# Kernel optimization log

Measured on AMD Instinct MI355X. Metric: run time of the kernel, lower is better.

Reference implementation:

```python
import jax, jax.numpy as jnp
import numpy as np

NEG_SLOPE = 0.2  # PyG GATConv default


def gat_conv(x, src, dst, W, att_src, att_dst, bias, n_nodes):
    # x: [N, F_in]; W: [F_in, H*C]; att_*: [H, C]; bias: [H*C]
    H, C = att_src.shape
    h = (x @ W).reshape(n_nodes, H, C)                      # [N, H, C]
    a_src = jnp.sum(h * att_src, axis=-1)                   # [N, H]
    a_dst = jnp.sum(h * att_dst, axis=-1)                   # [N, H]
    e = jax.nn.leaky_relu(a_src[src] + a_dst[dst], NEG_SLOPE)  # [E, H]
    # segment softmax over incoming edges of each dst node
    e_max = jax.ops.segment_max(e, dst, num_segments=n_nodes)
    e_max = jnp.where(jnp.isfinite(e_max), e_max, 0.0)
    ex = jnp.exp(e - e_max[dst])                             # [E, H]
    denom = jax.ops.segment_sum(ex, dst, num_segments=n_nodes)
    alpha = ex / (denom[dst] + 1e-16)                        # [E, H]
    msg = h[src] * alpha[:, :, None]                         # [E, H, C]
    out = jax.ops.segment_sum(msg, dst, num_segments=n_nodes)  # [N, H, C]
    return out.reshape(n_nodes, H * C) + bias


def setup_inputs() -> dict:
    key = jax.random.key(0)
    ks = jax.random.split(key, 12)
    N, F_in, Hd, heads, F_out, E = 50000, 128, 32, 8, 16, 800000
    x = jax.random.normal(ks[0], (N, F_in), dtype=jnp.float32)
    edge_index = jax.random.randint(ks[1], (2, E), 0, N, dtype=jnp.int64)
    g = 0.1
    return {
        "x": x,
        "edge_index": edge_index,
        "W1": jax.random.normal(ks[2], (F_in, heads * Hd), dtype=jnp.float32) * g,
        "att_src1": jax.random.normal(ks[3], (heads, Hd), dtype=jnp.float32) * g,
        "att_dst1": jax.random.normal(ks[4], (heads, Hd), dtype=jnp.float32) * g,
        "b1": jnp.zeros((heads * Hd,), dtype=jnp.float32),
        "W2": jax.random.normal(ks[5], (heads * Hd, Hd), dtype=jnp.float32) * g,
        "att_src2": jax.random.normal(ks[6], (1, Hd), dtype=jnp.float32) * g,
        "att_dst2": jax.random.normal(ks[7], (1, Hd), dtype=jnp.float32) * g,
        "b2": jnp.zeros((Hd,), dtype=jnp.float32),
        "Wout": jax.random.normal(ks[8], (Hd, F_out), dtype=jnp.float32) * g,
        "bout": jnp.zeros((F_out,), dtype=jnp.float32),
    }


def reference(x, edge_index, W1, att_src1, att_dst1, b1, W2, att_src2, att_dst2, b2, Wout, bout):
    N = x.shape[0]
    # PyG GATConv adds self loops by default
    loops = jnp.arange(N, dtype=edge_index.dtype)
    src = jnp.concatenate([edge_index[0], loops])
    dst = jnp.concatenate([edge_index[1], loops])
    h = jax.nn.elu(gat_conv(x, src, dst, W1, att_src1, att_dst1, b1, N))
    # dropout is identity in eval mode
    h = jax.nn.elu(gat_conv(h, src, dst, W2, att_src2, att_dst2, b2, N))
    return h @ Wout + bout
```

## Files before the change

kernel.cpp:

```cpp
#include <hip/hip_runtime.h>
#include <math.h>

#define NEG_SLOPE 0.2f

typedef __attribute__((ext_vector_type(8))) short bfrag8;
typedef __attribute__((ext_vector_type(4))) float f4acc;

__device__ __forceinline__ float bflo(unsigned int u) {
  union { unsigned int i; float f; } c;
  c.i = u << 16;
  return c.f;
}
__device__ __forceinline__ float bfhi(unsigned int u) {
  union { unsigned int i; float f; } c;
  c.i = u & 0xFFFF0000u;
  return c.f;
}
__device__ __forceinline__ unsigned short f2bf(float f) {
  union { float f; unsigned int i; } c;
  c.f = f;
  unsigned int i = c.i;
  return (unsigned short)((i + 0x7FFFu + ((i >> 16) & 1u)) >> 16);
}
__device__ __forceinline__ float elu(float x) { return x > 0.f ? x : __expf(x) - 1.f; }


__global__ __launch_bounds__(256) void prep_kernel(const int* __restrict__ ei,
                                                   int* __restrict__ counts,
                                                   const float* __restrict__ x,
                                                   const float* __restrict__ W1,
                                                   const float* __restrict__ W2,
                                                   unsigned short* __restrict__ xb,
                                                   unsigned short* __restrict__ w1t,
                                                   unsigned short* __restrict__ w2t,
                                                   int e, int xThreads, int totalx) {
  int gid = blockIdx.x * 256 + threadIdx.x;
  if (gid < e) {
    atomicAdd(&counts[ei[e + gid]], 1);
    return;
  }
  int g1 = gid - e;
  if (g1 < xThreads) {
    int i = g1 * 8;
    if (i < totalx) {
      float4 v0 = *(const float4*)(x + i);
      float4 v1 = *(const float4*)(x + i + 4);
      uint4 q;
      q.x = (unsigned int)f2bf(v0.x) | ((unsigned int)f2bf(v0.y) << 16);
      q.y = (unsigned int)f2bf(v0.z) | ((unsigned int)f2bf(v0.w) << 16);
      q.z = (unsigned int)f2bf(v1.x) | ((unsigned int)f2bf(v1.y) << 16);
      q.w = (unsigned int)f2bf(v1.z) | ((unsigned int)f2bf(v1.w) << 16);
      *(uint4*)(xb + i) = q;
    }
    return;
  }
  int g2 = g1 - xThreads;
#pragma unroll
  for (int u = 0; u < 4; ++u) {
    int j = g2 * 4 + u;
    if (j < 128 * 256) {
      int k = j >> 8, c = j & 255;
      w1t[c * 128 + k] = f2bf(W1[j]);
    } else if (j < 128 * 256 + 256 * 32) {
      int j2 = j - 128 * 256;
      int k = j2 >> 5, c = j2 & 31;
      w2t[c * 256 + k] = f2bf(W2[j2]);
    }
  }
}


#define SCAN_TILE 2048
__global__ __launch_bounds__(256) void scan_kernel(const int* __restrict__ counts,
                                                   int* __restrict__ offsets,
                                                   int* __restrict__ cursor,
                                                   int* __restrict__ bsum,
                                                   int* __restrict__ done,
                                                   int n, int nb) {
  __shared__ int wtot[4];
  __shared__ int preS, totS;
  int tid = threadIdx.x;
  int b = blockIdx.x;
  int base = b * SCAN_TILE + tid * 8;
  int v[8];
#pragma unroll
  for (int k = 0; k < 8; ++k) v[k] = (base + k < n) ? counts[base + k] + 1 : 0;
#pragma unroll
  for (int k = 1; k < 8; ++k) v[k] += v[k - 1];
  int tsum = v[7];
  int lane = tid & 63, w = tid >> 6;
  int ws = tsum;
#pragma unroll
  for (int off = 1; off < 64; off <<= 1) {
    int t = __shfl_up(ws, off, 64);
    if (lane >= off) ws += t;
  }
  if (lane == 63) wtot[w] = ws;
  __syncthreads();
  int woff = 0;
#pragma unroll
  for (int k = 0; k < 3; ++k)
    if (k < w) woff += wtot[k];
  int thrExcl = woff + ws - tsum;
  int blockTot = wtot[0] + wtot[1] + wtot[2] + wtot[3];

  if (tid == 0) {
    atomicExch(&bsum[b], blockTot);
    atomicAdd(done, 1);
    while (atomicAdd(done, 0) < nb) {
    }
    int pre = 0, tot = 0;
    for (int k = 0; k < nb; ++k) {
      int t = atomicAdd(&bsum[k], 0);
      if (k < b) pre += t;
      tot += t;
    }
    preS = pre;
    totS = tot;
  }
  __syncthreads();
  int pre = preS;
#pragma unroll
  for (int k = 0; k < 8; ++k) {
    int i = base + k;
    if (i < n) {
      int excl = pre + thrExcl + (k ? v[k - 1] : 0);
      offsets[i] = excl;
      cursor[i] = excl;
    }
  }
  if (b == 0 && tid == 0) offsets[n] = totS;
}


__global__ __launch_bounds__(256) void fillgemm1_kernel(
    const int* __restrict__ ei, int* __restrict__ cursor, int* __restrict__ csr,
    const unsigned short* __restrict__ xb, const unsigned short* __restrict__ w1t,
    const float* __restrict__ att_src, const float* __restrict__ att_dst,
    unsigned short* __restrict__ h1b, float* __restrict__ as1, float* __restrict__ ad1,
    int n, int e, int gBlocksX) {
  int bid = blockIdx.x;
  int gBlocks = gBlocksX * 2;
  if (bid >= gBlocks) {
    int i = (bid - gBlocks) * 256 + threadIdx.x;
    if (i < e) {
      int s = ei[i];
      int d = ei[e + i];
      int pos = atomicAdd(&cursor[d], 1);
      csr[pos] = s;
    } else if (i < e + n) {
      int node = i - e;
      int pos = atomicAdd(&cursor[node], 1);
      csr[pos] = node;
    } else if (i < e + n + 64) {
      csr[i] = 0;
    }
    return;
  }
  int bx = bid % gBlocksX, by = bid / gBlocksX;
  int tid = threadIdx.x;
  int wave = tid >> 6, lane = tid & 63;
  int quad = lane >> 4, l16 = lane & 15;
  int row0 = bx * 64 + wave * 16;
  int col0 = by * 128;
  int rowA = min(row0 + l16, n - 1);

  f4acc acc[8];
#pragma unroll
  for (int t = 0; t < 8; ++t) acc[t] = (f4acc)(0.f);

#pragma unroll
  for (int kc = 0; kc < 4; ++kc) {
    bfrag8 a = *(const bfrag8*)(xb + (size_t)rowA * 128 + kc * 32 + quad * 8);
#pragma unroll
    for (int t = 0; t < 8; ++t) {
      bfrag8 b = *(const bfrag8*)(w1t + (size_t)(col0 + t * 16 + l16) * 128 + kc * 32 + quad * 8);
      acc[t] = __builtin_amdgcn_mfma_f32_16x16x32_bf16(a, b, acc[t], 0, 0, 0);
    }
  }

#pragma unroll
  for (int r = 0; r < 4; ++r) {
    int gr = row0 + quad * 4 + r;
    if (gr < n) {
#pragma unroll
      for (int t = 0; t < 8; ++t)
        h1b[(size_t)gr * 256 + col0 + t * 16 + l16] = f2bf(acc[t][r]);
    }
  }

  float s1[4][4], s2[4][4];
#pragma unroll
  for (int r = 0; r < 4; ++r)
#pragma unroll
    for (int hl = 0; hl < 4; ++hl) { s1[r][hl] = 0.f; s2[r][hl] = 0.f; }
#pragma unroll
  for (int t = 0; t < 8; ++t) {
    float av = att_src[col0 + t * 16 + l16];
    float dv = att_dst[col0 + t * 16 + l16];
    int hl = t >> 1;
#pragma unroll
    for (int r = 0; r < 4; ++r) {
      s1[r][hl] += acc[t][r] * av;
      s2[r][hl] += acc[t][r] * dv;
    }
  }
#pragma unroll
  for (int r = 0; r < 4; ++r) {
#pragma unroll
    for (int hl = 0; hl < 4; ++hl) {
      float v1 = s1[r][hl], v2 = s2[r][hl];
      v1 += __shfl_xor(v1, 1); v1 += __shfl_xor(v1, 2);
      v1 += __shfl_xor(v1, 4); v1 += __shfl_xor(v1, 8);
      v2 += __shfl_xor(v2, 1); v2 += __shfl_xor(v2, 2);
      v2 += __shfl_xor(v2, 4); v2 += __shfl_xor(v2, 8);
      if (l16 == 0) {
        int gr = row0 + quad * 4 + r;
        if (gr < n) {
          int hg = (col0 >> 5) + hl;
          as1[(size_t)gr * 8 + hg] = v1;
          ad1[(size_t)gr * 8 + hg] = v2;
        }
      }
    }
  }
}


__global__ __launch_bounds__(256) void agg1_kernel(const unsigned short* __restrict__ h1b,
                                                   const float* __restrict__ as1,
                                                   const float* __restrict__ ad1,
                                                   const int* __restrict__ offsets,
                                                   const int* __restrict__ csr,
                                                   const float* __restrict__ bias,
                                                   unsigned short* __restrict__ h1ob, int n) {
  __shared__ float peLds[4 * 64 * 8];
  int gtid = blockIdx.x * 256 + threadIdx.x;
  int node = gtid >> 6;
  int lane = gtid & 63;
  if (node >= n) return;
  float* myPe = peLds + (threadIdx.x >> 6) * 512;
  int beg = offsets[node], end = offsets[node + 1];
  int deg = end - beg;
  int half = lane >> 5, sub = lane & 31, head = sub >> 2;

  float4 adv0 = ((const float4*)(ad1 + (size_t)node * 8))[0];
  float4 adv1 = ((const float4*)(ad1 + (size_t)node * 8))[1];
  float ad_[8] = {adv0.x, adv0.y, adv0.z, adv0.w, adv1.x, adv1.y, adv1.z, adv1.w};

  float l = 0.f;
  float a[8] = {};

  for (int c0 = 0; c0 < deg; c0 += 64) {
    int cnt = min(64, deg - c0);
    bool valid = (c0 + lane) < deg;
    int sreg = csr[beg + c0 + lane];
    {
      const float4* ap = (const float4*)(as1 + (size_t)sreg * 8);
      float4 r0 = ap[0], r1 = ap[1];
      float asv[8] = {r0.x, r0.y, r0.z, r0.w, r1.x, r1.y, r1.z, r1.w};
      float pv[8];
#pragma unroll
      for (int h = 0; h < 8; ++h) {
        float ev = asv[h] + ad_[h];
        ev = ev > 0.f ? ev : NEG_SLOPE * ev;
        pv[h] = valid ? __expf(ev) : 0.f;
      }
      *(float4*)&myPe[lane * 8 + 0] = make_float4(pv[0], pv[1], pv[2], pv[3]);
      *(float4*)&myPe[lane * 8 + 4] = make_float4(pv[4], pv[5], pv[6], pv[7]);
    }
#pragma unroll 8
    for (int j = 0; j < cnt; j += 2) {
      int e2 = j + half;
      int s2 = __shfl(sreg, e2);
      float pe = myPe[e2 * 8 + head];
      l += pe;
      uint4 hv = *(const uint4*)(h1b + (size_t)s2 * 256 + sub * 8);
      a[0] += pe * bflo(hv.x);
      a[1] += pe * bfhi(hv.x);
      a[2] += pe * bflo(hv.y);
      a[3] += pe * bfhi(hv.y);
      a[4] += pe * bflo(hv.z);
      a[5] += pe * bfhi(hv.z);
      a[6] += pe * bflo(hv.w);
      a[7] += pe * bfhi(hv.w);
    }
  }
  l += __shfl_xor(l, 32);
#pragma unroll
  for (int i = 0; i < 8; ++i) a[i] += __shfl_xor(a[i], 32);

  if (half == 0) {
    float inv = 1.f / (l + 1e-16f);
    const float4* bp = (const float4*)(bias + sub * 8);
    float4 b0 = bp[0], b1 = bp[1];
    float o[8];
    o[0] = elu(a[0] * inv + b0.x);
    o[1] = elu(a[1] * inv + b0.y);
    o[2] = elu(a[2] * inv + b0.z);
    o[3] = elu(a[3] * inv + b0.w);
    o[4] = elu(a[4] * inv + b1.x);
    o[5] = elu(a[5] * inv + b1.y);
    o[6] = elu(a[6] * inv + b1.z);
    o[7] = elu(a[7] * inv + b1.w);
    unsigned int q[4];
#pragma unroll
    for (int j = 0; j < 4; ++j)
      q[j] = (unsigned int)f2bf(o[j * 2]) | ((unsigned int)f2bf(o[j * 2 + 1]) << 16);
    *(uint4*)(h1ob + (size_t)node * 256 + sub * 8) = make_uint4(q[0], q[1], q[2], q[3]);
  }
}


__global__ __launch_bounds__(256) void gemm2_kernel(const unsigned short* __restrict__ h1ob,
                                                    const unsigned short* __restrict__ w2t,
                                                    const float* __restrict__ att_src,
                                                    const float* __restrict__ att_dst,
                                                    unsigned short* __restrict__ h2b,
                                                    float* __restrict__ as2,
                                                    float* __restrict__ ad2, int n) {
  int tid = threadIdx.x;
  int wave = tid >> 6, lane = tid & 63;
  int quad = lane >> 4, l16 = lane & 15;
  int row0 = blockIdx.x * 64 + wave * 16;
  int rowA = min(row0 + l16, n - 1);

  f4acc acc[2];
  acc[0] = (f4acc)(0.f);
  acc[1] = (f4acc)(0.f);

#pragma unroll
  for (int kc = 0; kc < 8; ++kc) {
    bfrag8 a = *(const bfrag8*)(h1ob + (size_t)rowA * 256 + kc * 32 + quad * 8);
#pragma unroll
    for (int t = 0; t < 2; ++t) {
      bfrag8 b = *(const bfrag8*)(w2t + (size_t)(t * 16 + l16) * 256 + kc * 32 + quad * 8);
      acc[t] = __builtin_amdgcn_mfma_f32_16x16x32_bf16(a, b, acc[t], 0, 0, 0);
    }
  }

#pragma unroll
  for (int r = 0; r < 4; ++r) {
    int gr = row0 + quad * 4 + r;
    if (gr < n) {
      h2b[(size_t)gr * 32 + l16] = f2bf(acc[0][r]);
      h2b[(size_t)gr * 32 + 16 + l16] = f2bf(acc[1][r]);
    }
  }

  float s1[4], s2v[4];
#pragma unroll
  for (int r = 0; r < 4; ++r) { s1[r] = 0.f; s2v[r] = 0.f; }
#pragma unroll
  for (int t = 0; t < 2; ++t) {
    float av = att_src[t * 16 + l16];
    float dv = att_dst[t * 16 + l16];
#pragma unroll
    for (int r = 0; r < 4; ++r) {
      s1[r] += acc[t][r] * av;
      s2v[r] += acc[t][r] * dv;
    }
  }
#pragma unroll
  for (int r = 0; r < 4; ++r) {
    float v1 = s1[r], v2 = s2v[r];
    v1 += __shfl_xor(v1, 1); v1 += __shfl_xor(v1, 2);
    v1 += __shfl_xor(v1, 4); v1 += __shfl_xor(v1, 8);
    v2 += __shfl_xor(v2, 1); v2 += __shfl_xor(v2, 2);
    v2 += __shfl_xor(v2, 4); v2 += __shfl_xor(v2, 8);
    if (l16 == 0) {
      int gr = row0 + quad * 4 + r;
      if (gr < n) {
        as2[gr] = v1;
        ad2[gr] = v2;
      }
    }
  }
}


__global__ __launch_bounds__(256) void agg2_kernel(const unsigned short* __restrict__ h2b,
                                                   const float* __restrict__ as2,
                                                   const float* __restrict__ ad2,
                                                   const int* __restrict__ offsets,
                                                   const int* __restrict__ csr,
                                                   const float* __restrict__ bias,
                                                   const float* __restrict__ Wout,
                                                   const float* __restrict__ bout,
                                                   float* __restrict__ out, int n) {
  __shared__ float peLds[4 * 64];
  __shared__ float wLds[512];
  __shared__ float hrow[4][32];
  int tid = threadIdx.x;
  wLds[tid] = Wout[tid];
  wLds[tid + 256] = Wout[tid + 256];
  __syncthreads();

  int gtid = blockIdx.x * 256 + tid;
  int node = gtid >> 6;
  int lane = gtid & 63;
  if (node >= n) return;
  int wv = tid >> 6;
  float* myPe = peLds + wv * 64;
  float ad = ad2[node];
  int beg = offsets[node], end = offsets[node + 1];
  int deg = end - beg;
  int quarter = lane >> 4;
  int dsub = lane & 15;

  float l = 0.f, a0 = 0.f, a1 = 0.f;
  for (int c0 = 0; c0 < deg; c0 += 64) {
    int cnt = min(64, deg - c0);
    bool valid = (c0 + lane) < deg;
    int sreg = csr[beg + c0 + lane];
    float ev = as2[sreg] + ad;
    ev = ev > 0.f ? ev : NEG_SLOPE * ev;
    myPe[lane] = valid ? __expf(ev) : 0.f;
#pragma unroll 8
    for (int j = 0; j < cnt; j += 4) {
      int e2 = j + quarter;
      int s2 = __shfl(sreg, e2);
      float pe = myPe[e2];
      l += pe;
      unsigned int hv = *(const unsigned int*)(h2b + (size_t)s2 * 32 + dsub * 2);
      a0 += pe * bflo(hv);
      a1 += pe * bfhi(hv);
    }
  }
  l += __shfl_xor(l, 16);
  l += __shfl_xor(l, 32);
  a0 += __shfl_xor(a0, 16);
  a1 += __shfl_xor(a1, 16);
  a0 += __shfl_xor(a0, 32);
  a1 += __shfl_xor(a1, 32);
  if (lane < 16) {
    float inv = 1.f / (l + 1e-16f);
    float o0 = elu(a0 * inv + bias[dsub * 2]);
    float o1 = elu(a1 * inv + bias[dsub * 2 + 1]);
    hrow[wv][dsub * 2] = o0;
    hrow[wv][dsub * 2 + 1] = o1;
  }
  if (lane < 16) {
    float s = bout[lane];
#pragma unroll
    for (int c = 0; c < 32; ++c) s += hrow[wv][c] * wLds[c * 16 + lane];
    out[(size_t)node * 16 + lane] = s;
  }
}


extern "C" void kernel_launch(void* const* d_in, const int* in_sizes, int n_in,
                              void* d_out, int out_size, void* d_ws, size_t ws_size,
                              hipStream_t stream) {
  const float* x        = (const float*)d_in[0];
  const int*   ei       = (const int*)d_in[1];
  const float* W1       = (const float*)d_in[2];
  const float* att_src1 = (const float*)d_in[3];
  const float* att_dst1 = (const float*)d_in[4];
  const float* b1       = (const float*)d_in[5];
  const float* W2       = (const float*)d_in[6];
  const float* att_src2 = (const float*)d_in[7];
  const float* att_dst2 = (const float*)d_in[8];
  const float* b2       = (const float*)d_in[9];
  const float* Wout     = (const float*)d_in[10];
  const float* bout     = (const float*)d_in[11];
  float* out = (float*)d_out;

  int n = in_sizes[0] / 128;
  int e = in_sizes[1] / 2;

  char* w = (char*)d_ws;
  unsigned short* h1b  = (unsigned short*)w; w += (size_t)n * 256 * 2;
  unsigned short* h1ob = (unsigned short*)w; w += (size_t)n * 256 * 2;
  unsigned short* xb   = (unsigned short*)w; w += (size_t)n * 128 * 2;
  unsigned short* h2b  = (unsigned short*)w; w += (size_t)n * 32 * 2;
  unsigned short* w1t  = (unsigned short*)w; w += (size_t)256 * 128 * 2;
  unsigned short* w2t  = (unsigned short*)w; w += (size_t)32 * 256 * 2;
  float* as1  = (float*)w; w += (size_t)n * 8 * 4;
  float* ad1  = (float*)w; w += (size_t)n * 8 * 4;
  float* as2  = (float*)w; w += (size_t)n * 4;
  float* ad2  = (float*)w; w += (size_t)n * 4;
  int* counts  = (int*)w; w += (size_t)n * 4;
  int* done    = (int*)w; w += (size_t)16 * 4;
  int* offsets = (int*)w; w += (size_t)(n + 16) * 4;
  int* cursor  = (int*)w; w += (size_t)n * 4;
  int* csr     = (int*)w; w += (size_t)(e + n + 64) * 4;
  int* bsum    = (int*)w; w += (size_t)256 * 4;

  int nb = (n + SCAN_TILE - 1) / SCAN_TILE;

  hipMemsetAsync(counts, 0, (size_t)(n + 16) * 4, stream);

  int xThreads = (n * 128 + 7) / 8;
  int prepThreads = e + xThreads + (128 * 256 + 256 * 32 + 3) / 4;
  prep_kernel<<<(prepThreads + 255) / 256, 256, 0, stream>>>(ei, counts, x, W1, W2,
                                                             xb, w1t, w2t, e, xThreads,
                                                             n * 128);

  scan_kernel<<<nb, 256, 0, stream>>>(counts, offsets, cursor, bsum, done, n, nb);

  int gBlocksX = (n + 63) / 64;
  int gBlocks = gBlocksX * 2;
  int fillBlocks = (e + n + 64 + 255) / 256;
  fillgemm1_kernel<<<gBlocks + fillBlocks, 256, 0, stream>>>(
      ei, cursor, csr, xb, w1t, att_src1, att_dst1, h1b, as1, ad1, n, e, gBlocksX);

  agg1_kernel<<<(n + 3) / 4, 256, 0, stream>>>(h1b, as1, ad1, offsets, csr, b1, h1ob, n);

  gemm2_kernel<<<(n + 63) / 64, 256, 0, stream>>>(h1ob, w2t, att_src2, att_dst2,
                                                  h2b, as2, ad2, n);
  agg2_kernel<<<(n + 3) / 4, 256, 0, stream>>>(h2b, as2, ad2, offsets, csr, b2,
                                               Wout, bout, out, n);
}
```

Before: 336.0 us.

## Fuse layer-2 GEMM into agg1 and convert x to bf16 inside GEMM1

The separate x-to-bf16 pass and the W2 transpose are removed. GEMM1 now reads fp32 x and converts it to bf16 in registers. The layer-2 projection, along with its attention scores, is computed at the end of agg1: each wave stages its ELU output row in LDS and multiplies it by a bf16 copy of W2 held in LDS, so the h1ob intermediate and the gemm2 launch go away. In exchange, every agg1 block reloads and converts all of W2 into LDS, uses more shared memory (which may lower occupancy), and does the 256x32 projection with scalar FMAs instead of MFMA.

```diff
diff --git a/kernel.cpp b/kernel.cpp
--- a/kernel.cpp
+++ b/kernel.cpp
@@ -27,44 +27,21 @@
 
 __global__ __launch_bounds__(256) void prep_kernel(const int* __restrict__ ei,
                                                    int* __restrict__ counts,
-                                                   const float* __restrict__ x,
                                                    const float* __restrict__ W1,
-                                                   const float* __restrict__ W2,
-                                                   unsigned short* __restrict__ xb,
                                                    unsigned short* __restrict__ w1t,
-                                                   unsigned short* __restrict__ w2t,
-                                                   int e, int xThreads, int totalx) {
+                                                   int e) {
   int gid = blockIdx.x * 256 + threadIdx.x;
   if (gid < e) {
     atomicAdd(&counts[ei[e + gid]], 1);
     return;
   }
-  int g1 = gid - e;
-  if (g1 < xThreads) {
-    int i = g1 * 8;
-    if (i < totalx) {
-      float4 v0 = *(const float4*)(x + i);
-      float4 v1 = *(const float4*)(x + i + 4);
-      uint4 q;
-      q.x = (unsigned int)f2bf(v0.x) | ((unsigned int)f2bf(v0.y) << 16);
-      q.y = (unsigned int)f2bf(v0.z) | ((unsigned int)f2bf(v0.w) << 16);
-      q.z = (unsigned int)f2bf(v1.x) | ((unsigned int)f2bf(v1.y) << 16);
-      q.w = (unsigned int)f2bf(v1.z) | ((unsigned int)f2bf(v1.w) << 16);
-      *(uint4*)(xb + i) = q;
-    }
-    return;
-  }
-  int g2 = g1 - xThreads;
+  int g2 = gid - e;
 #pragma unroll
   for (int u = 0; u < 4; ++u) {
     int j = g2 * 4 + u;
     if (j < 128 * 256) {
       int k = j >> 8, c = j & 255;
       w1t[c * 128 + k] = f2bf(W1[j]);
-    } else if (j < 128 * 256 + 256 * 32) {
-      int j2 = j - 128 * 256;
-      int k = j2 >> 5, c = j2 & 31;
-      w2t[c * 256 + k] = f2bf(W2[j2]);
     }
   }
 }
@@ -135,14 +112,13 @@
 
 __global__ __launch_bounds__(256) void fillgemm1_kernel(
     const int* __restrict__ ei, int* __restrict__ cursor, int* __restrict__ csr,
-    const unsigned short* __restrict__ xb, const unsigned short* __restrict__ w1t,
+    const float* __restrict__ x, const unsigned short* __restrict__ w1t,
     const float* __restrict__ att_src, const float* __restrict__ att_dst,
     unsigned short* __restrict__ h1b, float* __restrict__ as1, float* __restrict__ ad1,
-    int n, int e, int gBlocksX) {
+    int n, int e, int fillBlocks, int gBlocksX) {
   int bid = blockIdx.x;
-  int gBlocks = gBlocksX * 2;
-  if (bid >= gBlocks) {
-    int i = (bid - gBlocks) * 256 + threadIdx.x;
+  if (bid < fillBlocks) {
+    int i = bid * 256 + threadIdx.x;
     if (i < e) {
       int s = ei[i];
       int d = ei[e + i];
@@ -157,7 +133,8 @@
     }
     return;
   }
-  int bx = bid % gBlocksX, by = bid / gBlocksX;
+  int gb = bid - fillBlocks;
+  int bx = gb % gBlocksX, by = gb / gBlocksX;
   int tid = threadIdx.x;
   int wave = tid >> 6, lane = tid & 63;
   int quad = lane >> 4, l16 = lane & 15;
@@ -171,7 +148,17 @@
 
 #pragma unroll
   for (int kc = 0; kc < 4; ++kc) {
-    bfrag8 a = *(const bfrag8*)(xb + (size_t)rowA * 128 + kc * 32 + quad * 8);
+    float4 a0 = *(const float4*)(x + (size_t)rowA * 128 + kc * 32 + quad * 8);
+    float4 a1 = *(const float4*)(x + (size_t)rowA * 128 + kc * 32 + quad * 8 + 4);
+    bfrag8 a;
+    a[0] = (short)f2bf(a0.x);
+    a[1] = (short)f2bf(a0.y);
+    a[2] = (short)f2bf(a0.z);
+    a[3] = (short)f2bf(a0.w);
+    a[4] = (short)f2bf(a1.x);
+    a[5] = (short)f2bf(a1.y);
+    a[6] = (short)f2bf(a1.z);
+    a[7] = (short)f2bf(a1.w);
 #pragma unroll
     for (int t = 0; t < 8; ++t) {
       bfrag8 b = *(const bfrag8*)(w1t + (size_t)(col0 + t * 16 + l16) * 128 + kc * 32 + quad * 8);
@@ -233,13 +220,28 @@
                                                    const int* __restrict__ offsets,
                                                    const int* __restrict__ csr,
                                                    const float* __restrict__ bias,
-                                                   unsigned short* __restrict__ h1ob, int n) {
+                                                   const float* __restrict__ W2,
+                                                   const float* __restrict__ att_src2,
+                                                   const float* __restrict__ att_dst2,
+                                                   unsigned short* __restrict__ h2b,
+                                                   float* __restrict__ as2,
+                                                   float* __restrict__ ad2, int n) {
   __shared__ float peLds[4 * 64 * 8];
-  int gtid = blockIdx.x * 256 + threadIdx.x;
+  __shared__ unsigned short w2b[256 * 34];
+  __shared__ float hrow[4][256];
+  int tid = threadIdx.x;
+  for (int t = tid; t < 8192; t += 256) {
+    int c = t >> 5, col = t & 31;
+    w2b[c * 34 + col] = f2bf(W2[t]);
+  }
+  __syncthreads();
+
+  int gtid = blockIdx.x * 256 + tid;
   int node = gtid >> 6;
   int lane = gtid & 63;
   if (node >= n) return;
-  float* myPe = peLds + (threadIdx.x >> 6) * 512;
+  int wv = tid >> 6;
+  float* myPe = peLds + wv * 512;
   int beg = offsets[node], end = offsets[node + 1];
   int deg = end - beg;
   int half = lane >> 5, sub = lane & 31, head = sub >> 2;
@@ -294,86 +296,38 @@
     float inv = 1.f / (l + 1e-16f);
     const float4* bp = (const float4*)(bias + sub * 8);
     float4 b0 = bp[0], b1 = bp[1];
-    float o[8];
-    o[0] = elu(a[0] * inv + b0.x);
-    o[1] = elu(a[1] * inv + b0.y);
-    o[2] = elu(a[2] * inv + b0.z);
-    o[3] = elu(a[3] * inv + b0.w);
-    o[4] = elu(a[4] * inv + b1.x);
-    o[5] = elu(a[5] * inv + b1.y);
-    o[6] = elu(a[6] * inv + b1.z);
-    o[7] = elu(a[7] * inv + b1.w);
-    unsigned int q[4];
-#pragma unroll
-    for (int j = 0; j < 4; ++j)
-      q[j] = (unsigned int)f2bf(o[j * 2]) | ((unsigned int)f2bf(o[j * 2 + 1]) << 16);
-    *(uint4*)(h1ob + (size_t)node * 256 + sub * 8) = make_uint4(q[0], q[1], q[2], q[3]);
-  }
-}
-
-
-__global__ __launch_bounds__(256) void gemm2_kernel(const unsigned short* __restrict__ h1ob,
-                                                    const unsigned short* __restrict__ w2t,
-                                                    const float* __restrict__ att_src,
-                                                    const float* __restrict__ att_dst,
-                                                    unsigned short* __restrict__ h2b,
-                                                    float* __restrict__ as2,
-                                                    float* __restrict__ ad2, int n) {
-  int tid = threadIdx.x;
-  int wave = tid >> 6, lane = tid & 63;
-  int quad = lane >> 4, l16 = lane & 15;
-  int row0 = blockIdx.x * 64 + wave * 16;
-  int rowA = min(row0 + l16, n - 1);
-
-  f4acc acc[2];
-  acc[0] = (f4acc)(0.f);
-  acc[1] = (f4acc)(0.f);
-
-#pragma unroll
-  for (int kc = 0; kc < 8; ++kc) {
-    bfrag8 a = *(const bfrag8*)(h1ob + (size_t)rowA * 256 + kc * 32 + quad * 8);
-#pragma unroll
-    for (int t = 0; t < 2; ++t) {
-      bfrag8 b = *(const bfrag8*)(w2t + (size_t)(t * 16 + l16) * 256 + kc * 32 + quad * 8);
-      acc[t] = __builtin_amdgcn_mfma_f32_16x16x32_bf16(a, b, acc[t], 0, 0, 0);
-    }
-  }
-
-#pragma unroll
-  for (int r = 0; r < 4; ++r) {
-    int gr = row0 + quad * 4 + r;
-    if (gr < n) {
-      h2b[(size_t)gr * 32 + l16] = f2bf(acc[0][r]);
-      h2b[(size_t)gr * 32 + 16 + l16] = f2bf(acc[1][r]);
-    }
-  }
-
-  float s1[4], s2v[4];
-#pragma unroll
-  for (int r = 0; r < 4; ++r) { s1[r] = 0.f; s2v[r] = 0.f; }
-#pragma unroll
-  for (int t = 0; t < 2; ++t) {
-    float av = att_src[t * 16 + l16];
-    float dv = att_dst[t * 16 + l16];
-#pragma unroll
-    for (int r = 0; r < 4; ++r) {
-      s1[r] += acc[t][r] * av;
-      s2v[r] += acc[t][r] * dv;
-    }
-  }
-#pragma unroll
-  for (int r = 0; r < 4; ++r) {
-    float v1 = s1[r], v2 = s2v[r];
-    v1 += __shfl_xor(v1, 1); v1 += __shfl_xor(v1, 2);
-    v1 += __shfl_xor(v1, 4); v1 += __shfl_xor(v1, 8);
-    v2 += __shfl_xor(v2, 1); v2 += __shfl_xor(v2, 2);
-    v2 += __shfl_xor(v2, 4); v2 += __shfl_xor(v2, 8);
-    if (l16 == 0) {
-      int gr = row0 + quad * 4 + r;
-      if (gr < n) {
-        as2[gr] = v1;
-        ad2[gr] = v2;
-      }
+    float* hr = &hrow[wv][sub * 8];
+    hr[0] = elu(a[0] * inv + b0.x);
+    hr[1] = elu(a[1] * inv + b0.y);
+    hr[2] = elu(a[2] * inv + b0.z);
+    hr[3] = elu(a[3] * inv + b0.w);
+    hr[4] = elu(a[4] * inv + b1.x);
+    hr[5] = elu(a[5] * inv + b1.y);
+    hr[6] = elu(a[6] * inv + b1.z);
+    hr[7] = elu(a[7] * inv + b1.w);
+  }
+  int col = lane & 31, ch = lane >> 5;
+  const float* hr = hrow[wv];
+  float v = 0.f;
+  for (int c0 = ch * 128; c0 < ch * 128 + 128; c0 += 8) {
+#pragma unroll
+    for (int k = 0; k < 8; ++k)
+      v += hr[c0 + k] * bflo((unsigned int)w2b[(c0 + k) * 34 + col]);
+  }
+  v += __shfl_xor(v, 32);
+  if (lane < 32) {
+    h2b[(size_t)node * 32 + col] = f2bf(v);
+    float sa = v * att_src2[col];
+    float sd = v * att_dst2[col];
+    sa += __shfl_xor(sa, 1); sa += __shfl_xor(sa, 2);
+    sa += __shfl_xor(sa, 4); sa += __shfl_xor(sa, 8);
+    sa += __shfl_xor(sa, 16);
+    sd += __shfl_xor(sd, 1); sd += __shfl_xor(sd, 2);
+    sd += __shfl_xor(sd, 4); sd += __shfl_xor(sd, 8);
+    sd += __shfl_xor(sd, 16);
+    if (lane == 0) {
+      as2[node] = sa;
+      ad2[node] = sd;
     }
   }
 }
@@ -471,11 +425,8 @@
 
   char* w = (char*)d_ws;
   unsigned short* h1b  = (unsigned short*)w; w += (size_t)n * 256 * 2;
-  unsigned short* h1ob = (unsigned short*)w; w += (size_t)n * 256 * 2;
-  unsigned short* xb   = (unsigned short*)w; w += (size_t)n * 128 * 2;
   unsigned short* h2b  = (unsigned short*)w; w += (size_t)n * 32 * 2;
   unsigned short* w1t  = (unsigned short*)w; w += (size_t)256 * 128 * 2;
-  unsigned short* w2t  = (unsigned short*)w; w += (size_t)32 * 256 * 2;
   float* as1  = (float*)w; w += (size_t)n * 8 * 4;
   float* ad1  = (float*)w; w += (size_t)n * 8 * 4;
   float* as2  = (float*)w; w += (size_t)n * 4;
@@ -491,24 +442,21 @@
 
   hipMemsetAsync(counts, 0, (size_t)(n + 16) * 4, stream);
 
-  int xThreads = (n * 128 + 7) / 8;
-  int prepThreads = e + xThreads + (128 * 256 + 256 * 32 + 3) / 4;
-  prep_kernel<<<(prepThreads + 255) / 256, 256, 0, stream>>>(ei, counts, x, W1, W2,
-                                                             xb, w1t, w2t, e, xThreads,
-                                                             n * 128);
+  int prepThreads = e + (128 * 256 + 3) / 4;
+  prep_kernel<<<(prepThreads + 255) / 256, 256, 0, stream>>>(ei, counts, W1, w1t, e);
 
   scan_kernel<<<nb, 256, 0, stream>>>(counts, offsets, cursor, bsum, done, n, nb);
 
+  int fillBlocks = (e + n + 64 + 255) / 256;
   int gBlocksX = (n + 63) / 64;
-  int gBlocks = gBlocksX * 2;
-  int fillBlocks = (e + n + 64 + 255) / 256;
-  fillgemm1_kernel<<<gBlocks + fillBlocks, 256, 0, stream>>>(
-      ei, cursor, csr, xb, w1t, att_src1, att_dst1, h1b, as1, ad1, n, e, gBlocksX);
-
-  agg1_kernel<<<(n + 3) / 4, 256, 0, stream>>>(h1b, as1, ad1, offsets, csr, b1, h1ob, n);
-
-  gemm2_kernel<<<(n + 63) / 64, 256, 0, stream>>>(h1ob, w2t, att_src2, att_dst2,
-                                                  h2b, as2, ad2, n);
+  int gemmBlocks = gBlocksX * 2;
+  fillgemm1_kernel<<<fillBlocks + gemmBlocks, 256, 0, stream>>>(
+      ei, cursor, csr, x, w1t, att_src1, att_dst1, h1b, as1, ad1, n, e, fillBlocks,
+      gBlocksX);
+
+  agg1_kernel<<<(n + 3) / 4, 256, 0, stream>>>(h1b, as1, ad1, offsets, csr, b1,
+                                               W2, att_src2, att_dst2, h2b, as2, ad2, n);
+
   agg2_kernel<<<(n + 3) / 4, 256, 0, stream>>>(h2b, as2, ad2, offsets, csr, b2,
                                                Wout, bout, out, n);
 }
```

New measurement: 375.5 us. 1.12x slower.

## Convert x to bf16 inside GEMM1, split fill from GEMM, stage h1 stores via LDS

Applied to the files above, without the earlier changes.

Drops the separate x-to-bf16 conversion pass in prep and its workspace buffer, so GEMM1 reads fp32 x directly and converts it in registers. The combined fill+GEMM launch is split into a CSR fill kernel and a standalone 2D-grid GEMM1 kernel. GEMM1 output is staged through shared memory so h1 is written with 16-byte row-contiguous stores instead of scattered 2-byte stores. This trades the extra bf16 copy round trip for double-size x reads in the GEMM, and it gives up the overlap between fill and GEMM in exchange for one more launch.

```diff
diff --git a/kernel.cpp b/kernel.cpp
--- a/kernel.cpp
+++ b/kernel.cpp
@@ -27,34 +27,17 @@
 
 __global__ __launch_bounds__(256) void prep_kernel(const int* __restrict__ ei,
                                                    int* __restrict__ counts,
-                                                   const float* __restrict__ x,
                                                    const float* __restrict__ W1,
                                                    const float* __restrict__ W2,
-                                                   unsigned short* __restrict__ xb,
                                                    unsigned short* __restrict__ w1t,
                                                    unsigned short* __restrict__ w2t,
-                                                   int e, int xThreads, int totalx) {
+                                                   int e) {
   int gid = blockIdx.x * 256 + threadIdx.x;
   if (gid < e) {
     atomicAdd(&counts[ei[e + gid]], 1);
     return;
   }
-  int g1 = gid - e;
-  if (g1 < xThreads) {
-    int i = g1 * 8;
-    if (i < totalx) {
-      float4 v0 = *(const float4*)(x + i);
-      float4 v1 = *(const float4*)(x + i + 4);
-      uint4 q;
-      q.x = (unsigned int)f2bf(v0.x) | ((unsigned int)f2bf(v0.y) << 16);
-      q.y = (unsigned int)f2bf(v0.z) | ((unsigned int)f2bf(v0.w) << 16);
-      q.z = (unsigned int)f2bf(v1.x) | ((unsigned int)f2bf(v1.y) << 16);
-      q.w = (unsigned int)f2bf(v1.z) | ((unsigned int)f2bf(v1.w) << 16);
-      *(uint4*)(xb + i) = q;
-    }
-    return;
-  }
-  int g2 = g1 - xThreads;
+  int g2 = gid - e;
 #pragma unroll
   for (int u = 0; u < 4; ++u) {
     int j = g2 * 4 + u;
@@ -132,37 +115,38 @@
   if (b == 0 && tid == 0) offsets[n] = totS;
 }
 
-
-__global__ __launch_bounds__(256) void fillgemm1_kernel(
-    const int* __restrict__ ei, int* __restrict__ cursor, int* __restrict__ csr,
-    const unsigned short* __restrict__ xb, const unsigned short* __restrict__ w1t,
-    const float* __restrict__ att_src, const float* __restrict__ att_dst,
-    unsigned short* __restrict__ h1b, float* __restrict__ as1, float* __restrict__ ad1,
-    int n, int e, int gBlocksX) {
-  int bid = blockIdx.x;
-  int gBlocks = gBlocksX * 2;
-  if (bid >= gBlocks) {
-    int i = (bid - gBlocks) * 256 + threadIdx.x;
-    if (i < e) {
-      int s = ei[i];
-      int d = ei[e + i];
-      int pos = atomicAdd(&cursor[d], 1);
-      csr[pos] = s;
-    } else if (i < e + n) {
-      int node = i - e;
-      int pos = atomicAdd(&cursor[node], 1);
-      csr[pos] = node;
-    } else if (i < e + n + 64) {
-      csr[i] = 0;
-    }
-    return;
-  }
-  int bx = bid % gBlocksX, by = bid / gBlocksX;
+__global__ __launch_bounds__(256) void fill_kernel(const int* __restrict__ ei,
+                                                   int* __restrict__ cursor,
+                                                   int* __restrict__ csr, int n, int e) {
+  int i = blockIdx.x * 256 + threadIdx.x;
+  if (i < e) {
+    int s = ei[i];
+    int d = ei[e + i];
+    int pos = atomicAdd(&cursor[d], 1);
+    csr[pos] = s;
+  } else if (i < e + n) {
+    int node = i - e;
+    int pos = atomicAdd(&cursor[node], 1);
+    csr[pos] = node;
+  } else if (i < e + n + 64) {
+    csr[i] = 0;
+  }
+}
+
+
+__global__ __launch_bounds__(256) void gemm1_kernel(const float* __restrict__ x,
+                                                    const unsigned short* __restrict__ w1t,
+                                                    const float* __restrict__ att_src,
+                                                    const float* __restrict__ att_dst,
+                                                    unsigned short* __restrict__ h1b,
+                                                    float* __restrict__ as1,
+                                                    float* __restrict__ ad1, int n) {
+  __shared__ unsigned short stw[4][16][136];
   int tid = threadIdx.x;
   int wave = tid >> 6, lane = tid & 63;
   int quad = lane >> 4, l16 = lane & 15;
-  int row0 = bx * 64 + wave * 16;
-  int col0 = by * 128;
+  int row0 = blockIdx.x * 64 + wave * 16;
+  int col0 = blockIdx.y * 128;
   int rowA = min(row0 + l16, n - 1);
 
   f4acc acc[8];
@@ -171,7 +155,17 @@
 
 #pragma unroll
   for (int kc = 0; kc < 4; ++kc) {
-    bfrag8 a = *(const bfrag8*)(xb + (size_t)rowA * 128 + kc * 32 + quad * 8);
+    float4 a0 = *(const float4*)(x + (size_t)rowA * 128 + kc * 32 + quad * 8);
+    float4 a1 = *(const float4*)(x + (size_t)rowA * 128 + kc * 32 + quad * 8 + 4);
+    bfrag8 a;
+    a[0] = (short)f2bf(a0.x);
+    a[1] = (short)f2bf(a0.y);
+    a[2] = (short)f2bf(a0.z);
+    a[3] = (short)f2bf(a0.w);
+    a[4] = (short)f2bf(a1.x);
+    a[5] = (short)f2bf(a1.y);
+    a[6] = (short)f2bf(a1.z);
+    a[7] = (short)f2bf(a1.w);
 #pragma unroll
     for (int t = 0; t < 8; ++t) {
       bfrag8 b = *(const bfrag8*)(w1t + (size_t)(col0 + t * 16 + l16) * 128 + kc * 32 + quad * 8);
@@ -181,12 +175,19 @@
 
 #pragma unroll
   for (int r = 0; r < 4; ++r) {
-    int gr = row0 + quad * 4 + r;
-    if (gr < n) {
-#pragma unroll
-      for (int t = 0; t < 8; ++t)
-        h1b[(size_t)gr * 256 + col0 + t * 16 + l16] = f2bf(acc[t][r]);
-    }
+    int lr = quad * 4 + r;
+#pragma unroll
+    for (int t = 0; t < 8; ++t)
+      stw[wave][lr][t * 16 + l16] = f2bf(acc[t][r]);
+  }
+#pragma unroll
+  for (int j = 0; j < 4; ++j) {
+    int idx = j * 64 + lane;
+    int row = idx >> 4, part = idx & 15;
+    int gr = row0 + row;
+    if (gr < n)
+      *(uint4*)(h1b + (size_t)gr * 256 + col0 + part * 8) =
+          *(const uint4*)&stw[wave][row][part * 8];
   }
 
   float s1[4][4], s2[4][4];
@@ -472,7 +473,6 @@
   char* w = (char*)d_ws;
   unsigned short* h1b  = (unsigned short*)w; w += (size_t)n * 256 * 2;
   unsigned short* h1ob = (unsigned short*)w; w += (size_t)n * 256 * 2;
-  unsigned short* xb   = (unsigned short*)w; w += (size_t)n * 128 * 2;
   unsigned short* h2b  = (unsigned short*)w; w += (size_t)n * 32 * 2;
   unsigned short* w1t  = (unsigned short*)w; w += (size_t)256 * 128 * 2;
   unsigned short* w2t  = (unsigned short*)w; w += (size_t)32 * 256 * 2;
@@ -491,20 +491,16 @@
 
   hipMemsetAsync(counts, 0, (size_t)(n + 16) * 4, stream);
 
-  int xThreads = (n * 128 + 7) / 8;
-  int prepThreads = e + xThreads + (128 * 256 + 256 * 32 + 3) / 4;
-  prep_kernel<<<(prepThreads + 255) / 256, 256, 0, stream>>>(ei, counts, x, W1, W2,
-                                                             xb, w1t, w2t, e, xThreads,
-                                                             n * 128);
+  int prepThreads = e + (128 * 256 + 256 * 32 + 3) / 4;
+  prep_kernel<<<(prepThreads + 255) / 256, 256, 0, stream>>>(ei, counts, W1, W2,
+                                                             w1t, w2t, e);
 
   scan_kernel<<<nb, 256, 0, stream>>>(counts, offsets, cursor, bsum, done, n, nb);
 
-  int gBlocksX = (n + 63) / 64;
-  int gBlocks = gBlocksX * 2;
-  int fillBlocks = (e + n + 64 + 255) / 256;
-  fillgemm1_kernel<<<gBlocks + fillBlocks, 256, 0, stream>>>(
-      ei, cursor, csr, xb, w1t, att_src1, att_dst1, h1b, as1, ad1, n, e, gBlocksX);
-
+  fill_kernel<<<(e + n + 64 + 255) / 256, 256, 0, stream>>>(ei, cursor, csr, n, e);
+
+  gemm1_kernel<<<dim3((n + 63) / 64, 2), 256, 0, stream>>>(x, w1t, att_src1, att_dst1,
+                                                           h1b, as1, ad1, n);
   agg1_kernel<<<(n + 3) / 4, 256, 0, stream>>>(h1b, as1, ad1, offsets, csr, b1, h1ob, n);
 
   gemm2_kernel<<<(n + 63) / 64, 256, 0, stream>>>(h1ob, w2t, att_src2, att_dst2,
```

Result: no change. 340.9 us (+1.5%).
